# Optimization experiments

Measured on AMD Instinct MI355X. Metric: run time of the kernel, lower is better.

Reference implementation:

```python
import jax, jax.numpy as jnp
import numpy as np
from jax.scipy.special import logsumexp

TAU = 0.07
LAMBDA_LL = 1.0
LAMBDA_GL = 0.5
LAMBDA_SMOOTH = 0.1
NEG_INF = -jnp.inf


def setup_inputs() -> dict:
    key = jax.random.key(0)
    k1, k2, k3, k4 = jax.random.split(key, 4)
    B, L, D, K = 16, 32, 256, 131072
    return {
        "z_t": jax.random.normal(k1, (B, L, D), dtype=jnp.float32),
        "g": jax.random.normal(k2, (B, D), dtype=jnp.float32),
        "va_values": jax.random.uniform(k3, (B, L, 2), dtype=jnp.float32),
        "memory_queue": jax.random.normal(k4, (K, D), dtype=jnp.float32),
    }


def _combined_loss(z_t, g, memory_queue):
    B, L, D = z_t.shape
    N = B * L
    z = z_t.reshape(N, D)

    # ---- Global-Local loss: anchor g[b], positive z_t[b,t], negatives = frames of other clips + queue
    sim_gz = (g @ z.T) / TAU                      # [B, N]
    pos_gl = sim_gz.reshape(B, B, L)[jnp.arange(B), jnp.arange(B)]  # [B, L]
    col_batch = jnp.arange(N) // L                # batch id of each frame column
    neg_gl = jnp.where(col_batch[None, :] == jnp.arange(B)[:, None], NEG_INF, sim_gz)  # [B, N]
    q_gl = (g @ memory_queue.T) / TAU             # [B, K]
    lse_neg_gl = jnp.logaddexp(logsumexp(neg_gl, axis=1), logsumexp(q_gl, axis=1))     # [B]
    loss_gl = jnp.mean(jnp.logaddexp(pos_gl, lse_neg_gl[:, None]) - pos_gl)

    # ---- Local-Local loss: anchor (b,t), positive (b,t+1), negatives = all other frames + queue
    anchor_idx = (jnp.arange(B)[:, None] * L + jnp.arange(L - 1)[None, :]).reshape(-1)  # [M]
    M = anchor_idx.shape[0]
    sim_zz = (z @ z.T) / TAU                      # [N, N]
    rows = sim_zz[anchor_idx]                     # [M, N]
    pos_ll = sim_zz[anchor_idx, anchor_idx + 1]   # [M]
    r = jnp.arange(M)
    neg_rows = rows.at[r, anchor_idx].set(NEG_INF).at[r, anchor_idx + 1].set(NEG_INF)
    q_ll = (z[anchor_idx] @ memory_queue.T) / TAU  # [M, K] -- dominant memory traffic
    lse_neg_ll = jnp.logaddexp(logsumexp(neg_rows, axis=1), logsumexp(q_ll, axis=1))
    loss_ll = jnp.mean(jnp.logaddexp(pos_ll, lse_neg_ll) - pos_ll)
    # NOTE: the VA-derived positive weight in the original code is applied after
    # the logits are built, so it has no effect on the loss; reproduced faithfully.

    # ---- Smoothness loss
    diff = z_t[:, 1:, :] - z_t[:, :-1, :]
    loss_smooth = jnp.mean(jnp.sum(diff * diff, axis=-1))

    total = LAMBDA_LL * loss_ll + LAMBDA_GL * loss_gl + LAMBDA_SMOOTH * loss_smooth
    return total


def reference(z_t, g, va_values, memory_queue):
    # va_values is unused by the effective math (see note in _combined_loss)
    return _combined_loss(z_t, g, memory_queue)
```

## Files before the change

kernel.cpp:

```cpp
#include <hip/hip_runtime.h>
#include <hip/hip_bf16.h>

#define D_ 256
#define NROWS_Z 512
#define NROWS 528
#define KQ 131072
#define NBLK 256
#define KC 512
#define SUBT 32
#define SCALE_A (14.285714285714286f * 1.4426950408889634f)
#define LN2 0.6931471805599453f

typedef __attribute__((ext_vector_type(8))) short short8;
typedef __attribute__((ext_vector_type(4))) float f32x4;

__device__ __forceinline__ float exp2fast(float x) {
  float r; asm("v_exp_f32 %0, %1" : "=v"(r) : "v"(x)); return r;
}
__device__ __forceinline__ float log2fast(float x) {
  float r; asm("v_log_f32 %0, %1" : "=v"(r) : "v"(x)); return r;
}

__device__ __forceinline__ short bf16r(float x) {
  union { float f; unsigned u; } c; c.f = x;
  unsigned r = (c.u + 0x7fffu + ((c.u >> 16) & 1u)) >> 16;
  return (short)r;
}

__device__ __forceinline__ void merge_ms(float& m, float& s, float m2, float s2) {
  float mm = fmaxf(m, m2);
  s = s * exp2fast(m - mm) + s2 * exp2fast(m2 - mm);
  m = mm;
}

__device__ __forceinline__ void upd(float& m, float& s, float v) {
  float d = v - m;
  if (d > 0.f) { s *= exp2fast(-d); m = v; d = 0.f; }
  s += exp2fast(d);
}

__device__ __forceinline__ short8 cvt8(float4 a, float4 b) {
  short8 v;
  v[0] = bf16r(a.x); v[1] = bf16r(a.y); v[2] = bf16r(a.z); v[3] = bf16r(a.w);
  v[4] = bf16r(b.x); v[5] = bf16r(b.y); v[6] = bf16r(b.z); v[7] = bf16r(b.w);
  return v;
}

__global__ void prep_kernel(const float* __restrict__ z, const float* __restrict__ g,
                            short* __restrict__ Abf, short* __restrict__ Zp,
                            float* __restrict__ smoothp) {
  const int r = blockIdx.x, d = threadIdx.x;
  const float v = (r < NROWS_Z) ? z[r * D_ + d] : g[(r - NROWS_Z) * D_ + d];
  Abf[r * D_ + d] = bf16r(v * SCALE_A);
  if (r < NROWS_Z) {
    Zp[r * D_ + d] = bf16r(v);
    float acc = 0.f;
    if ((r & 31) != 31) { const float dv = z[(r + 1) * D_ + d] - v; acc = dv * dv; }
#pragma unroll
    for (int mask = 1; mask < 64; mask <<= 1) acc += __shfl_xor(acc, mask);
    __shared__ float red[4];
    if ((d & 63) == 0) red[d >> 6] = acc;
    __syncthreads();
    if (d == 0) smoothp[r] = red[0] + red[1] + red[2] + red[3];
  }
}

__global__ __launch_bounds__(512, 2) void big_kernel(
    const float* __restrict__ queue, const short* __restrict__ Abf,
    float2* __restrict__ zpart, float2* __restrict__ gpart) {
  const int tid = threadIdx.x, blk = blockIdx.x;
  const int wid = tid >> 6, lane = tid & 63;
  const int l15 = lane & 15, l4 = lane >> 4;

  __shared__ __align__(16) char qs[2][16 * 512];
  __shared__ float2 gbuf[8 * 16];

  short8 afrag[4][8];
#pragma unroll
  for (int s = 0; s < 4; ++s) {
    const short* base = Abf + (wid * 64 + s * 16 + l15) * D_ + l4 * 8;
#pragma unroll
    for (int k = 0; k < 8; ++k) afrag[s][k] = *(const short8*)(base + k * 32);
  }
  const short* gbase = Abf + (NROWS_Z + l15) * D_ + l4 * 8;

  float mz[4][4], sz[4][4];
#pragma unroll
  for (int s = 0; s < 4; ++s)
#pragma unroll
    for (int r = 0; r < 4; ++r) { mz[s][r] = -1e30f; sz[s][r] = 0.f; }
  float mg[4], sg[4];
#pragma unroll
  for (int r = 0; r < 4; ++r) { mg[r] = -1e30f; sg[r] = 0.f; }

  const int srow = tid >> 5;
  const int sslot = tid & 31;
  const int woff = srow * 512 + (((sslot ^ srow) & 31) << 4);
  const float* qbase = queue + (size_t)(blk * KC + srow) * D_ + sslot * 8;

  float4 pa = *(const float4*)qbase;
  float4 pb = *(const float4*)(qbase + 4);
  *(short8*)(qs[0] + woff) = cvt8(pa, pb);
  __syncthreads();

  for (int st = 0; st < SUBT; ++st) {
    const int cur = st & 1;
    if (st + 1 < SUBT) {
      const float* qp = qbase + (st + 1) * (16 * D_);
      pa = *(const float4*)qp;
      pb = *(const float4*)(qp + 4);
    }

    const f32x4 fz = {0.f, 0.f, 0.f, 0.f};
    f32x4 acc[4];
#pragma unroll
    for (int s = 0; s < 4; ++s) acc[s] = fz;

    const char* qb = qs[cur];
#pragma unroll
    for (int k = 0; k < 8; ++k) {
      const short8 bf = *(const short8*)(qb + l15 * 512 + ((((k * 4 + l4) ^ l15) & 31) << 4));
#pragma unroll
      for (int s = 0; s < 4; ++s)
        acc[s] = __builtin_amdgcn_mfma_f32_16x16x32_bf16(afrag[s][k], bf, acc[s], 0, 0, 0);
    }

    const bool gdo = ((st & 7) == wid);
    f32x4 accg = fz;
    if (gdo) {
#pragma unroll
      for (int k = 0; k < 8; ++k) {
        const short8 bf = *(const short8*)(qb + l15 * 512 + ((((k * 4 + l4) ^ l15) & 31) << 4));
        const short8 ag = *(const short8*)(gbase + k * 32);
        accg = __builtin_amdgcn_mfma_f32_16x16x32_bf16(ag, bf, accg, 0, 0, 0);
      }
    }

    if (st + 1 < SUBT)
      *(short8*)(qs[cur ^ 1] + woff) = cvt8(pa, pb);

#pragma unroll
    for (int s = 0; s < 4; ++s)
#pragma unroll
      for (int r = 0; r < 4; ++r) upd(mz[s][r], sz[s][r], acc[s][r]);
    if (gdo) {
#pragma unroll
      for (int r = 0; r < 4; ++r) upd(mg[r], sg[r], accg[r]);
    }
    __syncthreads();
  }

#pragma unroll
  for (int s = 0; s < 4; ++s)
#pragma unroll
    for (int r = 0; r < 4; ++r) {
#pragma unroll
      for (int mask = 1; mask < 16; mask <<= 1) {
        const float om = __shfl_xor(mz[s][r], mask);
        const float os = __shfl_xor(sz[s][r], mask);
        merge_ms(mz[s][r], sz[s][r], om, os);
      }
    }
#pragma unroll
  for (int r = 0; r < 4; ++r) {
#pragma unroll
    for (int mask = 1; mask < 16; mask <<= 1) {
      const float om = __shfl_xor(mg[r], mask);
      const float os = __shfl_xor(sg[r], mask);
      merge_ms(mg[r], sg[r], om, os);
    }
  }

  if (l15 == 0) {
#pragma unroll
    for (int s = 0; s < 4; ++s)
#pragma unroll
      for (int r = 0; r < 4; ++r) {
        const int row = wid * 64 + s * 16 + l4 * 4 + r;
        zpart[row * NBLK + blk] = make_float2(mz[s][r], sz[s][r]);
      }
#pragma unroll
    for (int r = 0; r < 4; ++r)
      gbuf[wid * 16 + l4 * 4 + r] = make_float2(mg[r], sg[r]);
  }
  __syncthreads();
  if (tid < 16) {
    float m = gbuf[tid].x, s = gbuf[tid].y;
    for (int w = 1; w < 8; ++w) merge_ms(m, s, gbuf[w * 16 + tid].x, gbuf[w * 16 + tid].y);
    gpart[tid * NBLK + blk] = make_float2(m, s);
  }
}

__global__ __launch_bounds__(512) void zmm_kernel(
    const short* __restrict__ Abf, const short* __restrict__ Zp,
    float2* __restrict__ zcol, float* __restrict__ posll, float* __restrict__ posgl) {
  const int tid = threadIdx.x;
  const int wid = tid >> 6, lane = tid & 63;
  const int l15 = lane & 15, l4 = lane >> 4;
  const int r0 = blockIdx.x * 16;

  short8 af[8];
#pragma unroll
  for (int k = 0; k < 8; ++k)
    af[k] = *(const short8*)(Abf + (r0 + l15) * D_ + l4 * 8 + k * 32);

  float m[4], s[4];
#pragma unroll
  for (int r = 0; r < 4; ++r) { m[r] = -1e30f; s[r] = 0.f; }

  for (int st = 0; st < 4; ++st) {
    const int c0 = wid * 64 + st * 16;
    const f32x4 fz = {0.f, 0.f, 0.f, 0.f};
    f32x4 acc = fz;
#pragma unroll
    for (int k = 0; k < 8; ++k) {
      const short8 bq = *(const short8*)(Zp + (c0 + l15) * D_ + l4 * 8 + k * 32);
      acc = __builtin_amdgcn_mfma_f32_16x16x32_bf16(af[k], bq, acc, 0, 0, 0);
    }
#pragma unroll
    for (int r = 0; r < 4; ++r) {
      const int row = r0 + l4 * 4 + r;
      const int col = c0 + l15;
      const float v = acc[r];
      bool masked;
      if (r0 < NROWS_Z) {
        if (col == row + 1) posll[row] = v * LN2;
        masked = (col == row) || (col == row + 1);
      } else {
        const int b = row - NROWS_Z;
        const bool own = ((col >> 5) == b);
        if (own) posgl[col] = v * LN2;
        masked = own;
      }
      if (!masked) upd(m[r], s[r], v);
    }
  }
#pragma unroll
  for (int r = 0; r < 4; ++r) {
#pragma unroll
    for (int mask = 1; mask < 16; mask <<= 1) {
      const float om = __shfl_xor(m[r], mask);
      const float os = __shfl_xor(s[r], mask);
      merge_ms(m[r], s[r], om, os);
    }
  }
  __shared__ float2 lds[8][16];
  if (l15 == 0) {
#pragma unroll
    for (int r = 0; r < 4; ++r) lds[wid][l4 * 4 + r] = make_float2(m[r], s[r]);
  }
  __syncthreads();
  if (tid < 16) {
    float mm = lds[0][tid].x, ss = lds[0][tid].y;
    for (int w = 1; w < 8; ++w) merge_ms(mm, ss, lds[w][tid].x, lds[w][tid].y);
    zcol[r0 + tid] = make_float2(mm, ss);
  }
}

__global__ void reduce_kernel(const float2* __restrict__ zpart, const float2* __restrict__ gpart,
                              const float2* __restrict__ zcol, float* __restrict__ lse_row) {
  const int r = blockIdx.x, tid = threadIdx.x;
  const float2 p = (r < NROWS_Z) ? zpart[r * NBLK + tid] : gpart[(r - NROWS_Z) * NBLK + tid];
  float m = p.x, s = p.y;
  __shared__ float2 red[4];
#pragma unroll
  for (int mask = 1; mask < 64; mask <<= 1) {
    const float om = __shfl_xor(m, mask);
    const float os = __shfl_xor(s, mask);
    merge_ms(m, s, om, os);
  }
  if ((tid & 63) == 0) red[tid >> 6] = make_float2(m, s);
  __syncthreads();
  if (tid == 0) {
    for (int w = 1; w < 4; ++w) merge_ms(m, s, red[w].x, red[w].y);
    const float2 zc = zcol[r];
    merge_ms(m, s, zc.x, zc.y);
    lse_row[r] = LN2 * (m + log2fast(s));
  }
}

__global__ void final_kernel(const float* __restrict__ lse_row, const float* __restrict__ posll,
                             const float* __restrict__ posgl, const float* __restrict__ smoothp,
                             float* __restrict__ out) {
  const int tid = threadIdx.x;
  float a_ll = 0.f, a_gl = 0.f, a_sm = 0.f;
  for (int i = tid; i < 496; i += 256) {
    const int b = i / 31, t = i - b * 31;
    const int a = b * 32 + t;
    const float pos = posll[a], lse = lse_row[a];
    const float d = lse - pos;
    a_ll += (d > 0.f) ? d + log1pf(__expf(-d)) : log1pf(__expf(d));
  }
  for (int i = tid; i < 512; i += 256) {
    const float pos = posgl[i], lse = lse_row[NROWS_Z + (i >> 5)];
    const float d = lse - pos;
    a_gl += (d > 0.f) ? d + log1pf(__expf(-d)) : log1pf(__expf(d));
  }
  for (int i = tid; i < 512; i += 256) a_sm += smoothp[i];

  __shared__ float red[4];
  float sums[3] = {a_ll, a_gl, a_sm};
  float tot[3];
  for (int j = 0; j < 3; ++j) {
    float v = sums[j];
#pragma unroll
    for (int mask = 1; mask < 64; mask <<= 1) v += __shfl_xor(v, mask);
    __syncthreads();
    if ((tid & 63) == 0) red[tid >> 6] = v;
    __syncthreads();
    tot[j] = red[0] + red[1] + red[2] + red[3];
  }
  if (tid == 0)
    out[0] = tot[0] / 496.f + 0.5f * (tot[1] / 512.f) + 0.1f * (tot[2] / 496.f);
}

extern "C" void kernel_launch(void* const* d_in, const int* in_sizes, int n_in,
                              void* d_out, int out_size, void* d_ws, size_t ws_size,
                              hipStream_t stream) {
  const float* z = (const float*)d_in[0];
  const float* g = (const float*)d_in[1];
  const float* queue = (const float*)d_in[3];
  float* out = (float*)d_out;
  char* ws = (char*)d_ws;

  constexpr size_t OFF_A = 0;
  constexpr size_t OFF_ZP = OFF_A + 270336;
  constexpr size_t OFF_ZPART = OFF_ZP + 262144;
  constexpr size_t OFF_GPART = OFF_ZPART + 1048576;
  constexpr size_t OFF_ZCOL = OFF_GPART + 32768;
  constexpr size_t OFF_POSLL = OFF_ZCOL + 4224;
  constexpr size_t OFF_POSGL = OFF_POSLL + 2048;
  constexpr size_t OFF_SM = OFF_POSGL + 2048;
  constexpr size_t OFF_LSE = OFF_SM + 2048;

  short* Abf = (short*)(ws + OFF_A);
  short* Zp = (short*)(ws + OFF_ZP);
  float2* zpart = (float2*)(ws + OFF_ZPART);
  float2* gpart = (float2*)(ws + OFF_GPART);
  float2* zcol = (float2*)(ws + OFF_ZCOL);
  float* posll = (float*)(ws + OFF_POSLL);
  float* posgl = (float*)(ws + OFF_POSGL);
  float* smoothp = (float*)(ws + OFF_SM);
  float* lse_row = (float*)(ws + OFF_LSE);

  prep_kernel<<<NROWS, 256, 0, stream>>>(z, g, Abf, Zp, smoothp);
  big_kernel<<<NBLK, 512, 0, stream>>>(queue, Abf, zpart, gpart);
  zmm_kernel<<<33, 512, 0, stream>>>(Abf, Zp, zcol, posll, posgl);
  reduce_kernel<<<NROWS, 256, 0, stream>>>(zpart, gpart, zcol, lse_row);
  final_kernel<<<1, 256, 0, stream>>>(lse_row, posll, posgl, smoothp, out);
}
```

Before: 99.44 us.

## Deepen queue prefetch to two stages, lazy max rescale, packed bf16 convert

```diff
diff --git a/kernel.cpp b/kernel.cpp
--- a/kernel.cpp
+++ b/kernel.cpp
@@ -35,15 +35,21 @@
 
 __device__ __forceinline__ void upd(float& m, float& s, float v) {
   float d = v - m;
-  if (d > 0.f) { s *= exp2fast(-d); m = v; d = 0.f; }
+  if (__builtin_expect(__any(d > 8.f), 0)) {
+    const float mn = fmaxf(m, v);
+    s *= exp2fast(m - mn);
+    m = mn; d = v - m;
+  }
   s += exp2fast(d);
 }
 
 __device__ __forceinline__ short8 cvt8(float4 a, float4 b) {
-  short8 v;
-  v[0] = bf16r(a.x); v[1] = bf16r(a.y); v[2] = bf16r(a.z); v[3] = bf16r(a.w);
-  v[4] = bf16r(b.x); v[5] = bf16r(b.y); v[6] = bf16r(b.z); v[7] = bf16r(b.w);
-  return v;
+  union { unsigned u[4]; short8 s; } o;
+  asm("v_cvt_pk_bf16_f32 %0, %1, %2" : "=v"(o.u[0]) : "v"(a.x), "v"(a.y));
+  asm("v_cvt_pk_bf16_f32 %0, %1, %2" : "=v"(o.u[1]) : "v"(a.z), "v"(a.w));
+  asm("v_cvt_pk_bf16_f32 %0, %1, %2" : "=v"(o.u[2]) : "v"(b.x), "v"(b.y));
+  asm("v_cvt_pk_bf16_f32 %0, %1, %2" : "=v"(o.u[3]) : "v"(b.z), "v"(b.w));
+  return o.s;
 }
 
 __global__ void prep_kernel(const float* __restrict__ z, const float* __restrict__ g,
@@ -65,7 +71,9 @@
   }
 }
 
-__global__ __launch_bounds__(512, 2) void big_kernel(
+__global__ __launch_bounds__(512)
+__attribute__((amdgpu_waves_per_eu(2, 2)))
+void big_kernel(
     const float* __restrict__ queue, const short* __restrict__ Abf,
     float2* __restrict__ zpart, float2* __restrict__ gpart) {
   const int tid = threadIdx.x, blk = blockIdx.x;
@@ -98,54 +106,79 @@
   const int woff = srow * 512 + (((sslot ^ srow) & 31) << 4);
   const float* qbase = queue + (size_t)(blk * KC + srow) * D_ + sslot * 8;
 
-  float4 pa = *(const float4*)qbase;
-  float4 pb = *(const float4*)(qbase + 4);
-  *(short8*)(qs[0] + woff) = cvt8(pa, pb);
+  const f32x4 fz = {0.f, 0.f, 0.f, 0.f};
+
+  float4 fa0 = *(const float4*)qbase;
+  float4 fa1 = *(const float4*)(qbase + 4);
+  float4 fb0 = *(const float4*)(qbase + 16 * D_);
+  float4 fb1 = *(const float4*)(qbase + 16 * D_ + 4);
+  *(short8*)(qs[0] + woff) = cvt8(fa0, fa1);
   __syncthreads();
 
-  for (int st = 0; st < SUBT; ++st) {
-    const int cur = st & 1;
-    if (st + 1 < SUBT) {
-      const float* qp = qbase + (st + 1) * (16 * D_);
-      pa = *(const float4*)qp;
-      pb = *(const float4*)(qp + 4);
-    }
-
-    const f32x4 fz = {0.f, 0.f, 0.f, 0.f};
-    f32x4 acc[4];
-#pragma unroll
-    for (int s = 0; s < 4; ++s) acc[s] = fz;
-
-    const char* qb = qs[cur];
-#pragma unroll
-    for (int k = 0; k < 8; ++k) {
-      const short8 bf = *(const short8*)(qb + l15 * 512 + ((((k * 4 + l4) ^ l15) & 31) << 4));
-#pragma unroll
-      for (int s = 0; s < 4; ++s)
-        acc[s] = __builtin_amdgcn_mfma_f32_16x16x32_bf16(afrag[s][k], bf, acc[s], 0, 0, 0);
-    }
-
-    const bool gdo = ((st & 7) == wid);
-    f32x4 accg = fz;
-    if (gdo) {
-#pragma unroll
-      for (int k = 0; k < 8; ++k) {
-        const short8 bf = *(const short8*)(qb + l15 * 512 + ((((k * 4 + l4) ^ l15) & 31) << 4));
-        const short8 ag = *(const short8*)(gbase + k * 32);
-        accg = __builtin_amdgcn_mfma_f32_16x16x32_bf16(ag, bf, accg, 0, 0, 0);
-      }
-    }
-
-    if (st + 1 < SUBT)
-      *(short8*)(qs[cur ^ 1] + woff) = cvt8(pa, pb);
-
-#pragma unroll
-    for (int s = 0; s < 4; ++s)
-#pragma unroll
-      for (int r = 0; r < 4; ++r) upd(mz[s][r], sz[s][r], acc[s][r]);
-    if (gdo) {
-#pragma unroll
-      for (int r = 0; r < 4; ++r) upd(mg[r], sg[r], accg[r]);
+#define MFMA_BLOCK(BUF, ACC)                                                          \
+  {                                                                                   \
+    const char* qb = qs[BUF];                                                         \
+    _Pragma("unroll")                                                                 \
+    for (int k = 0; k < 8; ++k) {                                                     \
+      const short8 bf = *(const short8*)(qb + l15 * 512 + ((((k * 4 + l4) ^ l15) & 31) << 4)); \
+      _Pragma("unroll")                                                               \
+      for (int s = 0; s < 4; ++s)                                                     \
+        ACC[s] = __builtin_amdgcn_mfma_f32_16x16x32_bf16(afrag[s][k], bf, ACC[s], 0, 0, 0); \
+    }                                                                                 \
+  }
+
+#define G_BLOCK(BUF, ST)                                                              \
+  if (((ST) & 7) == wid) {                                                            \
+    const char* qb = qs[BUF];                                                         \
+    f32x4 accg = fz;                                                                  \
+    _Pragma("unroll")                                                                 \
+    for (int k = 0; k < 8; ++k) {                                                     \
+      const short8 bf = *(const short8*)(qb + l15 * 512 + ((((k * 4 + l4) ^ l15) & 31) << 4)); \
+      const short8 ag = *(const short8*)(gbase + k * 32);                             \
+      accg = __builtin_amdgcn_mfma_f32_16x16x32_bf16(ag, bf, accg, 0, 0, 0);          \
+    }                                                                                 \
+    _Pragma("unroll")                                                                 \
+    for (int r = 0; r < 4; ++r) upd(mg[r], sg[r], accg[r]);                           \
+  }
+
+#define UPD_BLOCK(ACC)                                                                \
+  _Pragma("unroll")                                                                   \
+  for (int s = 0; s < 4; ++s)                                                         \
+    _Pragma("unroll")                                                                 \
+    for (int r = 0; r < 4; ++r) upd(mz[s][r], sz[s][r], ACC[s][r]);
+
+  for (int st = 0; st < SUBT; st += 2) {
+    if (st + 2 < SUBT) {
+      const float* qp = qbase + (st + 2) * (16 * D_);
+      fa0 = *(const float4*)qp;
+      fa1 = *(const float4*)(qp + 4);
+    }
+    {
+      f32x4 acc[4];
+#pragma unroll
+      for (int s = 0; s < 4; ++s) acc[s] = fz;
+      MFMA_BLOCK(0, acc)
+      G_BLOCK(0, st)
+      UPD_BLOCK(acc)
+    }
+    *(short8*)(qs[1] + woff) = cvt8(fb0, fb1);
+    __syncthreads();
+
+    if (st + 3 < SUBT) {
+      const float* qp = qbase + (st + 3) * (16 * D_);
+      fb0 = *(const float4*)qp;
+      fb1 = *(const float4*)(qp + 4);
+    }
+    {
+      f32x4 acc[4];
+#pragma unroll
+      for (int s = 0; s < 4; ++s) acc[s] = fz;
+      MFMA_BLOCK(1, acc)
+      G_BLOCK(1, st + 1)
+      UPD_BLOCK(acc)
+    }
+    if (st + 2 < SUBT) {
+      *(short8*)(qs[0] + woff) = cvt8(fa0, fa1);
     }
     __syncthreads();
   }
```

Result: slower. 141.5 us (+42.3%).
